# Kernel optimization log

Hardware: AMD Instinct MI355X
Metric: run time of the kernel (lower is better)

## Reference

```python
import jax, jax.numpy as jnp
import numpy as np

DIM = 768
CA = 192  # int(dim * mlp_ratio)
T = 8

def setup_inputs() -> dict:
    key = jax.random.key(0)
    ks = jax.random.split(key, 7)
    x = jax.random.normal(ks[0], (197, 128, DIM), dtype=jnp.float32)
    w1 = jax.random.normal(ks[1], (DIM, CA), dtype=jnp.float32) * 0.02
    b1 = jax.random.normal(ks[2], (CA,), dtype=jnp.float32) * 0.02
    conv_w = jax.random.normal(ks[3], (CA, 3), dtype=jnp.float32) * 0.02  # depthwise temporal kernel (3,1,1)
    conv_b = jax.random.normal(ks[4], (CA,), dtype=jnp.float32) * 0.02
    w2 = jax.random.normal(ks[5], (CA, DIM), dtype=jnp.float32) * 0.02
    b2 = jax.random.normal(ks[6], (DIM,), dtype=jnp.float32) * 0.02
    return {"x": x, "w1": w1, "b1": b1, "conv_w": conv_w, "conv_b": conv_b, "w2": w2, "b2": b2}

def reference(x, w1, b1, conv_w, conv_b, w2, b2):
    # x: (L, BT, dim), tokens-first layout (fc1 applied before permute)
    x_id = x
    h = x @ w1 + b1                      # (L, BT, Ca)
    h = jnp.transpose(h, (1, 0, 2))      # (BT, L, Ca)
    BT, L, Ca = h.shape
    B = BT // T
    h = h[:, 1:, :]                      # drop first token (L-1 patch tokens)
    x_cls = h[:, :1, :]                  # (BT, 1, Ca) -- first token AFTER the slice (as in original)
    x_temp = h.reshape(B, T, L - 1, Ca)  # (B, T, P, Ca)
    # Depthwise Conv3d with kernel (3,1,1), pad (1,0,0): pure temporal depthwise conv.
    xp = jnp.pad(x_temp, ((0, 0), (1, 1), (0, 0), (0, 0)))
    x_after = (xp[:, :-2] * conv_w[:, 0] + xp[:, 1:-1] * conv_w[:, 1]
               + xp[:, 2:] * conv_w[:, 2] + conv_b)  # (B, T, P, Ca)
    # Triangular-masked pairwise diff: sum_{i<j} (x_after[j] - x_temp[i]) / 28,
    # computed without materializing the (B,T,T,P,Ca) diff tensor:
    # each x_after[j] appears j times; each x_temp[i] appears (T-1-i) times.
    t = jnp.arange(T, dtype=x.dtype)
    result = (jnp.einsum('t,btpc->bpc', t, x_after)
              - jnp.einsum('t,btpc->bpc', (T - 1) - t, x_temp)) / 28.0
    x_last = (x_temp + result[:, None]).reshape(BT, L - 1, Ca)
    out = jnp.concatenate([x_cls, x_last], axis=1)   # (BT, L, Ca)
    out = jnp.transpose(out, (1, 0, 2))              # (L, BT, Ca)
    out = jax.nn.gelu(out, approximate=False)        # torch nn.GELU default = exact erf
    out = out @ w2 + b2                              # (L, BT, dim)
    return x_id + out
```

## Files before the change

### kernel.cpp

```cpp
#include <hip/hip_runtime.h>
#include <hip/hip_bf16.h>
#include <math.h>

#define DIM   768
#define CA    192
#define NTOK  25216

typedef __attribute__((ext_vector_type(8))) short short8;
typedef __attribute__((ext_vector_type(4))) float f32x4;

static __device__ __forceinline__ short f2bf(float f) {
    union { __hip_bfloat16 b; short s; } u;
    u.b = __float2bfloat16(f);
    return u.s;
}
static __device__ __forceinline__ float gelu_exact(float x) {
    return 0.5f * x * (1.0f + erff(x * 0.70710678118654752440f));
}
static __device__ __forceinline__ void ld16(void* lds, const void* gsrc) {
    __builtin_amdgcn_global_load_lds((const __attribute__((address_space(1))) void*)gsrc,
                                     (__attribute__((address_space(3))) void*)lds, 16, 0, 0);
}

__global__ void prep_kernel(const float* __restrict__ w1, const float* __restrict__ w2,
                            short* __restrict__ w1T, short* __restrict__ w2T) {
    int idx = blockIdx.x * 256 + threadIdx.x;
    if (idx < CA * DIM) {
        int n = idx / DIM, k = idx - n * DIM;
        w1T[idx] = f2bf(w1[k * CA + n]);
        int n2 = idx / CA, k2 = idx - n2 * CA;
        w2T[idx] = f2bf(w2[k2 * DIM + n2]);
    }
}

__global__ __launch_bounds__(256) void gemm1_fused(
        const float* __restrict__ x, const short* __restrict__ w1T,
        const float* __restrict__ b1, const float* __restrict__ conv_w,
        const float* __restrict__ conv_b, short* __restrict__ gq) {
    __shared__ __align__(16) short As[64 * 40];
    __shared__ __align__(16) short Bs[2][96 * 32];

    const int tid = threadIdx.x;
    const int bx  = blockIdx.x;
    const int l   = (bx >> 2) + 1;
    const int hm  = (bx >> 1) & 1;
    const int n0  = (bx & 1) * 96;
    const int R0  = l * 128 + hm * 64;

    const int wave = tid >> 6, lane = tid & 63;
    const int wm = wave >> 1, wn = wave & 1;
    const int lm = lane & 15, lg = lane >> 4;
    const int lk = lg * 8;

    const int arow = tid >> 2;
    const int acol = (tid & 3) * 8;
    const float* xrow = x + (size_t)(R0 + arow) * DIM + acol;

    f32x4 acc[2][3] = {};

    f32x4 av0 = *(const f32x4*)(xrow);
    f32x4 av1 = *(const f32x4*)(xrow + 4);
    if (wave < 3) {
        #pragma unroll
        for (int j = 0; j < 2; j++) {
            int s = (wave * 2 + j) * 64 + lane;
            int m = s >> 2;
            int q = (s & 3) ^ ((m >> 1) & 3);
            ld16(&Bs[0][(wave * 2 + j) * 512], w1T + (size_t)(n0 + m) * DIM + q * 8);
        }
    }

    for (int i = 0; i < 24; i++) {
        const int p = i & 1;
        short8 a8;
        #pragma unroll
        for (int e = 0; e < 4; e++) { a8[e] = f2bf(av0[e]); a8[4 + e] = f2bf(av1[e]); }
        __syncthreads();
        *(short8*)&As[arow * 40 + acol] = a8;
        __syncthreads();
        if (i < 23) {
            const float* xn = xrow + (i + 1) * 32;
            av0 = *(const f32x4*)(xn);
            av1 = *(const f32x4*)(xn + 4);
            if (wave < 3) {
                const int k0n = (i + 1) * 32;
                #pragma unroll
                for (int j = 0; j < 2; j++) {
                    int s = (wave * 2 + j) * 64 + lane;
                    int m = s >> 2;
                    int q = (s & 3) ^ ((m >> 1) & 3);
                    ld16(&Bs[1 - p][(wave * 2 + j) * 512],
                         w1T + (size_t)(n0 + m) * DIM + k0n + q * 8);
                }
            }
        }
        short8 af[2], bf[3];
        af[0] = *(const short8*)&As[(wm * 32 + lm) * 40 + lk];
        af[1] = *(const short8*)&As[(wm * 32 + 16 + lm) * 40 + lk];
        #pragma unroll
        for (int j = 0; j < 3; j++) {
            int rB = wn * 48 + j * 16 + lm;
            int qs = lg ^ ((rB >> 1) & 3);
            bf[j] = *(const short8*)&Bs[p][rB * 32 + qs * 8];
        }
        #pragma unroll
        for (int i2 = 0; i2 < 2; i2++)
            #pragma unroll
            for (int j = 0; j < 3; j++)
                acc[i2][j] = __builtin_amdgcn_mfma_f32_16x16x32_bf16(af[i2], bf[j], acc[i2][j], 0, 0, 0);
    }

    const int g1 = lg & 1;
    #pragma unroll
    for (int j = 0; j < 3; j++) {
        const int c = n0 + wn * 48 + j * 16 + lm;
        const float b1c = b1[c];
        const float cw0 = conv_w[c * 3 + 0];
        const float cw1 = conv_w[c * 3 + 1];
        const float cw2 = conv_w[c * 3 + 2];
        const float cb  = conv_b[c];
        #pragma unroll
        for (int i2 = 0; i2 < 2; i2++) {
            float hv[4];
            #pragma unroll
            for (int r = 0; r < 4; r++) hv[r] = acc[i2][j][r] + b1c;
            float partial = 0.f;
            #pragma unroll
            for (int r = 0; r < 4; r++) {
                const int t = g1 * 4 + r;
                const float tf = (float)t;
                float coef = tf * cw1 - (7.0f - tf);
                if (t <= 6) coef += (tf + 1.0f) * cw0;
                if (t >= 1) coef += (tf - 1.0f) * cw2;
                partial += coef * hv[r];
            }
            const float full = partial + __shfl_xor(partial, 16);
            const float res = cb + full * (1.0f / 28.0f);
            const int row = R0 + wm * 32 + i2 * 16 + lg * 4;
            #pragma unroll
            for (int r = 0; r < 4; r++)
                gq[(size_t)(row + r) * CA + c] = f2bf(gelu_exact(hv[r] + res));
            if (l == 1) {
                const int bt = row - 128;
                #pragma unroll
                for (int r = 0; r < 4; r++)
                    gq[(size_t)(bt + r) * CA + c] = f2bf(gelu_exact(hv[r]));
            }
        }
    }
}

__global__ __launch_bounds__(256) void gemm2_kernel(
        const short* __restrict__ gq, const short* __restrict__ w2T,
        const float* __restrict__ b2, const float* __restrict__ x,
        float* __restrict__ out) {
    __shared__ __align__(16) short As[2][64 * 64];
    __shared__ __align__(16) short Bs[2][128 * 64];

    const int tid = threadIdx.x;
    const int m0 = blockIdx.x * 64;
    const int n0 = blockIdx.y * 128;
    const int wave = tid >> 6, lane = tid & 63;
    const int wm = wave >> 1, wn = wave & 1;
    const int lm = lane & 15, lg = lane >> 4;

    f32x4 acc[2][4] = {};

    #pragma unroll
    for (int j = 0; j < 2; j++) {
        int s = (wave * 2 + j) * 64 + lane;
        int m = s >> 3, q = (s & 7) ^ (m & 7);
        ld16(&As[0][(wave * 2 + j) * 512], gq + (size_t)(m0 + m) * CA + q * 8);
    }
    #pragma unroll
    for (int j = 0; j < 4; j++) {
        int s = (wave * 4 + j) * 64 + lane;
        int m = s >> 3, q = (s & 7) ^ (m & 7);
        ld16(&Bs[0][(wave * 4 + j) * 512], w2T + (size_t)(n0 + m) * CA + q * 8);
    }

    for (int i = 0; i < 3; i++) {
        const int p = i & 1;
        __syncthreads();
        if (i < 2) {
            const int k0 = (i + 1) * 64;
            #pragma unroll
            for (int j = 0; j < 2; j++) {
                int s = (wave * 2 + j) * 64 + lane;
                int m = s >> 3, q = (s & 7) ^ (m & 7);
                ld16(&As[1 - p][(wave * 2 + j) * 512], gq + (size_t)(m0 + m) * CA + k0 + q * 8);
            }
            #pragma unroll
            for (int j = 0; j < 4; j++) {
                int s = (wave * 4 + j) * 64 + lane;
                int m = s >> 3, q = (s & 7) ^ (m & 7);
                ld16(&Bs[1 - p][(wave * 4 + j) * 512], w2T + (size_t)(n0 + m) * CA + k0 + q * 8);
            }
        }
        #pragma unroll
        for (int kk = 0; kk < 2; kk++) {
            const int cb0 = kk * 4 + lg;
            short8 af[2], bf[4];
            #pragma unroll
            for (int i2 = 0; i2 < 2; i2++) {
                int r = wm * 32 + i2 * 16 + lm;
                af[i2] = *(const short8*)&As[p][r * 64 + (cb0 ^ (r & 7)) * 8];
            }
            #pragma unroll
            for (int j = 0; j < 4; j++) {
                int r = wn * 64 + j * 16 + lm;
                bf[j] = *(const short8*)&Bs[p][r * 64 + (cb0 ^ (r & 7)) * 8];
            }
            #pragma unroll
            for (int i2 = 0; i2 < 2; i2++)
                #pragma unroll
                for (int j = 0; j < 4; j++)
                    acc[i2][j] = __builtin_amdgcn_mfma_f32_16x16x32_bf16(af[i2], bf[j], acc[i2][j], 0, 0, 0);
        }
    }

    #pragma unroll
    for (int i2 = 0; i2 < 2; i2++) {
        const int row0 = m0 + wm * 32 + i2 * 16 + lg * 4;
        #pragma unroll
        for (int j = 0; j < 4; j++) {
            const int col = n0 + wn * 64 + j * 16 + lm;
            const float bias = b2[col];
            #pragma unroll
            for (int r = 0; r < 4; r++) {
                const size_t idx = (size_t)(row0 + r) * DIM + col;
                out[idx] = acc[i2][j][r] + x[idx] + bias;
            }
        }
    }
}

extern "C" void kernel_launch(void* const* d_in, const int* in_sizes, int n_in,
                              void* d_out, int out_size, void* d_ws, size_t ws_size,
                              hipStream_t stream) {
    (void)in_sizes; (void)n_in; (void)out_size; (void)ws_size;
    const float* x      = (const float*)d_in[0];
    const float* w1     = (const float*)d_in[1];
    const float* b1     = (const float*)d_in[2];
    const float* conv_w = (const float*)d_in[3];
    const float* conv_b = (const float*)d_in[4];
    const float* w2     = (const float*)d_in[5];
    const float* b2     = (const float*)d_in[6];
    float* out = (float*)d_out;

    char* ws = (char*)d_ws;
    short* g   = (short*)ws;
    short* w1T = (short*)(ws + 9682944);
    short* w2T = (short*)(ws + 9682944 + 294912);

    prep_kernel<<<(CA * DIM + 255) / 256, 256, 0, stream>>>(w1, w2, w1T, w2T);
    gemm1_fused<<<784, 256, 0, stream>>>(x, w1T, b1, conv_w, conv_b, g);
    gemm2_kernel<<<dim3(394, 6), 256, 0, stream>>>(g, w2T, b2, x, out);
}
```

Baseline: 196.3 us.

## Load GEMM operands straight from global into registers, dropping LDS staging

Both GEMM kernels stop staging A and B tiles through shared memory with barriers. Each lane now loads its MFMA fragments directly from global memory into registers, prefetching the next k-step one iteration ahead, and launch bounds request 4 blocks per CU. This removes the LDS round trips and __syncthreads overhead, but each wave re-reads data that was previously shared across waves, which raises global/L2 traffic and uses less coalesced access patterns.

```diff
diff --git a/kernel.cpp b/kernel.cpp
--- a/kernel.cpp
+++ b/kernel.cpp
@@ -16,10 +16,6 @@
 }
 static __device__ __forceinline__ float gelu_exact(float x) {
     return 0.5f * x * (1.0f + erff(x * 0.70710678118654752440f));
-}
-static __device__ __forceinline__ void ld16(void* lds, const void* gsrc) {
-    __builtin_amdgcn_global_load_lds((const __attribute__((address_space(1))) void*)gsrc,
-                                     (__attribute__((address_space(3))) void*)lds, 16, 0, 0);
 }
 
 __global__ void prep_kernel(const float* __restrict__ w1, const float* __restrict__ w2,
@@ -33,13 +29,10 @@
     }
 }
 
-__global__ __launch_bounds__(256) void gemm1_fused(
+__global__ __launch_bounds__(256, 4) void gemm1_fused(
         const float* __restrict__ x, const short* __restrict__ w1T,
         const float* __restrict__ b1, const float* __restrict__ conv_w,
         const float* __restrict__ conv_b, short* __restrict__ gq) {
-    __shared__ __align__(16) short As[64 * 40];
-    __shared__ __align__(16) short Bs[2][96 * 32];
-
     const int tid = threadIdx.x;
     const int bx  = blockIdx.x;
     const int l   = (bx >> 2) + 1;
@@ -50,64 +43,68 @@
     const int wave = tid >> 6, lane = tid & 63;
     const int wm = wave >> 1, wn = wave & 1;
     const int lm = lane & 15, lg = lane >> 4;
-    const int lk = lg * 8;
-
-    const int arow = tid >> 2;
-    const int acol = (tid & 3) * 8;
-    const float* xrow = x + (size_t)(R0 + arow) * DIM + acol;
+
+    const float* aBase0 = x + (size_t)(R0 + wm * 32 + lm) * DIM + lg * 8;
+    const float* aBase1 = aBase0 + (size_t)16 * DIM;
+    const short* bBase  = w1T + (size_t)(n0 + wn * 48 + lm) * DIM + lg * 8;
 
     f32x4 acc[2][3] = {};
 
-    f32x4 av0 = *(const f32x4*)(xrow);
-    f32x4 av1 = *(const f32x4*)(xrow + 4);
-    if (wave < 3) {
-        #pragma unroll
-        for (int j = 0; j < 2; j++) {
-            int s = (wave * 2 + j) * 64 + lane;
-            int m = s >> 2;
-            int q = (s & 3) ^ ((m >> 1) & 3);
-            ld16(&Bs[0][(wave * 2 + j) * 512], w1T + (size_t)(n0 + m) * DIM + q * 8);
-        }
-    }
-
-    for (int i = 0; i < 24; i++) {
-        const int p = i & 1;
-        short8 a8;
-        #pragma unroll
-        for (int e = 0; e < 4; e++) { a8[e] = f2bf(av0[e]); a8[4 + e] = f2bf(av1[e]); }
-        __syncthreads();
-        *(short8*)&As[arow * 40 + acol] = a8;
-        __syncthreads();
-        if (i < 23) {
-            const float* xn = xrow + (i + 1) * 32;
-            av0 = *(const f32x4*)(xn);
-            av1 = *(const f32x4*)(xn + 4);
-            if (wave < 3) {
-                const int k0n = (i + 1) * 32;
-                #pragma unroll
-                for (int j = 0; j < 2; j++) {
-                    int s = (wave * 2 + j) * 64 + lane;
-                    int m = s >> 2;
-                    int q = (s & 3) ^ ((m >> 1) & 3);
-                    ld16(&Bs[1 - p][(wave * 2 + j) * 512],
-                         w1T + (size_t)(n0 + m) * DIM + k0n + q * 8);
-                }
-            }
-        }
-        short8 af[2], bf[3];
-        af[0] = *(const short8*)&As[(wm * 32 + lm) * 40 + lk];
-        af[1] = *(const short8*)&As[(wm * 32 + 16 + lm) * 40 + lk];
-        #pragma unroll
-        for (int j = 0; j < 3; j++) {
-            int rB = wn * 48 + j * 16 + lm;
-            int qs = lg ^ ((rB >> 1) & 3);
-            bf[j] = *(const short8*)&Bs[p][rB * 32 + qs * 8];
+    f32x4 pa[2][2];
+    short8 pb[3];
+    pa[0][0] = *(const f32x4*)(aBase0);
+    pa[0][1] = *(const f32x4*)(aBase0 + 4);
+    pa[1][0] = *(const f32x4*)(aBase1);
+    pa[1][1] = *(const f32x4*)(aBase1 + 4);
+    pb[0] = *(const short8*)(bBase);
+    pb[1] = *(const short8*)(bBase + 16 * DIM);
+    pb[2] = *(const short8*)(bBase + 32 * DIM);
+
+    #pragma unroll
+    for (int i = 0; i < 23; i++) {
+        const int kn = (i + 1) * 32;
+        f32x4 na[2][2];
+        short8 nb[3];
+        na[0][0] = *(const f32x4*)(aBase0 + kn);
+        na[0][1] = *(const f32x4*)(aBase0 + kn + 4);
+        na[1][0] = *(const f32x4*)(aBase1 + kn);
+        na[1][1] = *(const f32x4*)(aBase1 + kn + 4);
+        nb[0] = *(const short8*)(bBase + kn);
+        nb[1] = *(const short8*)(bBase + 16 * DIM + kn);
+        nb[2] = *(const short8*)(bBase + 32 * DIM + kn);
+
+        short8 af[2];
+        #pragma unroll
+        for (int e = 0; e < 4; e++) {
+            af[0][e]     = f2bf(pa[0][0][e]);
+            af[0][4 + e] = f2bf(pa[0][1][e]);
+            af[1][e]     = f2bf(pa[1][0][e]);
+            af[1][4 + e] = f2bf(pa[1][1][e]);
         }
         #pragma unroll
         for (int i2 = 0; i2 < 2; i2++)
             #pragma unroll
             for (int j = 0; j < 3; j++)
-                acc[i2][j] = __builtin_amdgcn_mfma_f32_16x16x32_bf16(af[i2], bf[j], acc[i2][j], 0, 0, 0);
+                acc[i2][j] = __builtin_amdgcn_mfma_f32_16x16x32_bf16(af[i2], pb[j], acc[i2][j], 0, 0, 0);
+
+        pa[0][0] = na[0][0]; pa[0][1] = na[0][1];
+        pa[1][0] = na[1][0]; pa[1][1] = na[1][1];
+        pb[0] = nb[0]; pb[1] = nb[1]; pb[2] = nb[2];
+    }
+    {
+        short8 af[2];
+        #pragma unroll
+        for (int e = 0; e < 4; e++) {
+            af[0][e]     = f2bf(pa[0][0][e]);
+            af[0][4 + e] = f2bf(pa[0][1][e]);
+            af[1][e]     = f2bf(pa[1][0][e]);
+            af[1][4 + e] = f2bf(pa[1][1][e]);
+        }
+        #pragma unroll
+        for (int i2 = 0; i2 < 2; i2++)
+            #pragma unroll
+            for (int j = 0; j < 3; j++)
+                acc[i2][j] = __builtin_amdgcn_mfma_f32_16x16x32_bf16(af[i2], pb[j], acc[i2][j], 0, 0, 0);
     }
 
     const int g1 = lg & 1;
@@ -150,13 +147,10 @@
     }
 }
 
-__global__ __launch_bounds__(256) void gemm2_kernel(
+__global__ __launch_bounds__(256, 4) void gemm2_kernel(
         const short* __restrict__ gq, const short* __restrict__ w2T,
         const float* __restrict__ b2, const float* __restrict__ x,
         float* __restrict__ out) {
-    __shared__ __align__(16) short As[2][64 * 64];
-    __shared__ __align__(16) short Bs[2][128 * 64];
-
     const int tid = threadIdx.x;
     const int m0 = blockIdx.x * 64;
     const int n0 = blockIdx.y * 128;
@@ -164,60 +158,44 @@
     const int wm = wave >> 1, wn = wave & 1;
     const int lm = lane & 15, lg = lane >> 4;
 
+    const short* aBase = gq  + (size_t)(m0 + wm * 32 + lm) * CA + lg * 8;
+    const short* bBase = w2T + (size_t)(n0 + wn * 64 + lm) * CA + lg * 8;
+
     f32x4 acc[2][4] = {};
 
-    #pragma unroll
-    for (int j = 0; j < 2; j++) {
-        int s = (wave * 2 + j) * 64 + lane;
-        int m = s >> 3, q = (s & 7) ^ (m & 7);
-        ld16(&As[0][(wave * 2 + j) * 512], gq + (size_t)(m0 + m) * CA + q * 8);
-    }
-    #pragma unroll
-    for (int j = 0; j < 4; j++) {
-        int s = (wave * 4 + j) * 64 + lane;
-        int m = s >> 3, q = (s & 7) ^ (m & 7);
-        ld16(&Bs[0][(wave * 4 + j) * 512], w2T + (size_t)(n0 + m) * CA + q * 8);
-    }
-
-    for (int i = 0; i < 3; i++) {
-        const int p = i & 1;
-        __syncthreads();
-        if (i < 2) {
-            const int k0 = (i + 1) * 64;
-            #pragma unroll
-            for (int j = 0; j < 2; j++) {
-                int s = (wave * 2 + j) * 64 + lane;
-                int m = s >> 3, q = (s & 7) ^ (m & 7);
-                ld16(&As[1 - p][(wave * 2 + j) * 512], gq + (size_t)(m0 + m) * CA + k0 + q * 8);
-            }
-            #pragma unroll
-            for (int j = 0; j < 4; j++) {
-                int s = (wave * 4 + j) * 64 + lane;
-                int m = s >> 3, q = (s & 7) ^ (m & 7);
-                ld16(&Bs[1 - p][(wave * 4 + j) * 512], w2T + (size_t)(n0 + m) * CA + k0 + q * 8);
-            }
-        }
-        #pragma unroll
-        for (int kk = 0; kk < 2; kk++) {
-            const int cb0 = kk * 4 + lg;
-            short8 af[2], bf[4];
-            #pragma unroll
-            for (int i2 = 0; i2 < 2; i2++) {
-                int r = wm * 32 + i2 * 16 + lm;
-                af[i2] = *(const short8*)&As[p][r * 64 + (cb0 ^ (r & 7)) * 8];
-            }
-            #pragma unroll
-            for (int j = 0; j < 4; j++) {
-                int r = wn * 64 + j * 16 + lm;
-                bf[j] = *(const short8*)&Bs[p][r * 64 + (cb0 ^ (r & 7)) * 8];
-            }
-            #pragma unroll
-            for (int i2 = 0; i2 < 2; i2++)
-                #pragma unroll
-                for (int j = 0; j < 4; j++)
-                    acc[i2][j] = __builtin_amdgcn_mfma_f32_16x16x32_bf16(af[i2], bf[j], acc[i2][j], 0, 0, 0);
-        }
-    }
+    short8 pa[2], pb[4];
+    pa[0] = *(const short8*)(aBase);
+    pa[1] = *(const short8*)(aBase + 16 * CA);
+    pb[0] = *(const short8*)(bBase);
+    pb[1] = *(const short8*)(bBase + 16 * CA);
+    pb[2] = *(const short8*)(bBase + 32 * CA);
+    pb[3] = *(const short8*)(bBase + 48 * CA);
+
+    #pragma unroll
+    for (int i = 0; i < 5; i++) {
+        const int kn = (i + 1) * 32;
+        short8 na[2], nb[4];
+        na[0] = *(const short8*)(aBase + kn);
+        na[1] = *(const short8*)(aBase + 16 * CA + kn);
+        nb[0] = *(const short8*)(bBase + kn);
+        nb[1] = *(const short8*)(bBase + 16 * CA + kn);
+        nb[2] = *(const short8*)(bBase + 32 * CA + kn);
+        nb[3] = *(const short8*)(bBase + 48 * CA + kn);
+
+        #pragma unroll
+        for (int i2 = 0; i2 < 2; i2++)
+            #pragma unroll
+            for (int j = 0; j < 4; j++)
+                acc[i2][j] = __builtin_amdgcn_mfma_f32_16x16x32_bf16(pa[i2], pb[j], acc[i2][j], 0, 0, 0);
+
+        pa[0] = na[0]; pa[1] = na[1];
+        pb[0] = nb[0]; pb[1] = nb[1]; pb[2] = nb[2]; pb[3] = nb[3];
+    }
+    #pragma unroll
+    for (int i2 = 0; i2 < 2; i2++)
+        #pragma unroll
+        for (int j = 0; j < 4; j++)
+            acc[i2][j] = __builtin_amdgcn_mfma_f32_16x16x32_bf16(pa[i2], pb[j], acc[i2][j], 0, 0, 0);
 
     #pragma unroll
     for (int i2 = 0; i2 < 2; i2++) {
```

Result: slower. 255.4 us (+30.1%).

## Pre-convert x to bf16 and triple-buffer gemm1 with async LDS loads

Applied to the files above, without the earlier changes.

Adds a separate pass that converts x to bf16 into the output buffer, used as scratch. gemm1 can then stage both A and B tiles with global_load_lds in a 3-stage ring, using K=64 steps and fine-grained vmcnt waits. This replaces the in-register fp32->bf16 conversion and the double syncthreads per step. gemm2 gets a unified LDS ring with per-wave load assignment and a launch-bounds occupancy hint of 2. The cost is an extra full read of x and a write of a bf16 copy before gemm1, in exchange for better latency hiding.

```diff
diff --git a/kernel.cpp b/kernel.cpp
--- a/kernel.cpp
+++ b/kernel.cpp
@@ -33,12 +33,22 @@
     }
 }
 
-__global__ __launch_bounds__(256) void gemm1_fused(
-        const float* __restrict__ x, const short* __restrict__ w1T,
+__global__ __launch_bounds__(256) void xcvt_kernel(const float* __restrict__ x,
+                                                   short* __restrict__ xbf) {
+    size_t i = ((size_t)blockIdx.x * 256 + threadIdx.x) * 8;
+    f32x4 a = *(const f32x4*)(x + i);
+    f32x4 b = *(const f32x4*)(x + i + 4);
+    short8 o;
+    #pragma unroll
+    for (int e = 0; e < 4; e++) { o[e] = f2bf(a[e]); o[4 + e] = f2bf(b[e]); }
+    *(short8*)(xbf + i) = o;
+}
+
+__global__ __launch_bounds__(256, 2) void gemm1_fused(
+        const short* __restrict__ xbf, const short* __restrict__ w1T,
         const float* __restrict__ b1, const float* __restrict__ conv_w,
         const float* __restrict__ conv_b, short* __restrict__ gq) {
-    __shared__ __align__(16) short As[64 * 40];
-    __shared__ __align__(16) short Bs[2][96 * 32];
+    __shared__ __align__(16) short lds[3][10240];
 
     const int tid = threadIdx.x;
     const int bx  = blockIdx.x;
@@ -50,64 +60,71 @@
     const int wave = tid >> 6, lane = tid & 63;
     const int wm = wave >> 1, wn = wave & 1;
     const int lm = lane & 15, lg = lane >> 4;
-    const int lk = lg * 8;
-
-    const int arow = tid >> 2;
-    const int acol = (tid & 3) * 8;
-    const float* xrow = x + (size_t)(R0 + arow) * DIM + acol;
+
+    const short* src[5];
+    int loff[5];
+    #pragma unroll
+    for (int j = 0; j < 5; j++) {
+        int s5 = wave * 5 + j;
+        if (s5 < 8) {
+            int idx = s5 * 64 + lane;
+            int m = idx >> 3, q = (idx & 7) ^ (m & 7);
+            src[j]  = xbf + (size_t)(R0 + m) * DIM + q * 8;
+            loff[j] = s5 * 512;
+        } else {
+            int idx = (s5 - 8) * 64 + lane;
+            int m = idx >> 3, q = (idx & 7) ^ (m & 7);
+            src[j]  = w1T + (size_t)(n0 + m) * DIM + q * 8;
+            loff[j] = 4096 + (s5 - 8) * 512;
+        }
+    }
 
     f32x4 acc[2][3] = {};
 
-    f32x4 av0 = *(const f32x4*)(xrow);
-    f32x4 av1 = *(const f32x4*)(xrow + 4);
-    if (wave < 3) {
-        #pragma unroll
-        for (int j = 0; j < 2; j++) {
-            int s = (wave * 2 + j) * 64 + lane;
-            int m = s >> 2;
-            int q = (s & 3) ^ ((m >> 1) & 3);
-            ld16(&Bs[0][(wave * 2 + j) * 512], w1T + (size_t)(n0 + m) * DIM + q * 8);
-        }
-    }
-
-    for (int i = 0; i < 24; i++) {
-        const int p = i & 1;
-        short8 a8;
-        #pragma unroll
-        for (int e = 0; e < 4; e++) { a8[e] = f2bf(av0[e]); a8[4 + e] = f2bf(av1[e]); }
-        __syncthreads();
-        *(short8*)&As[arow * 40 + acol] = a8;
-        __syncthreads();
-        if (i < 23) {
-            const float* xn = xrow + (i + 1) * 32;
-            av0 = *(const f32x4*)(xn);
-            av1 = *(const f32x4*)(xn + 4);
-            if (wave < 3) {
-                const int k0n = (i + 1) * 32;
-                #pragma unroll
-                for (int j = 0; j < 2; j++) {
-                    int s = (wave * 2 + j) * 64 + lane;
-                    int m = s >> 2;
-                    int q = (s & 3) ^ ((m >> 1) & 3);
-                    ld16(&Bs[1 - p][(wave * 2 + j) * 512],
-                         w1T + (size_t)(n0 + m) * DIM + k0n + q * 8);
-                }
-            }
-        }
-        short8 af[2], bf[3];
-        af[0] = *(const short8*)&As[(wm * 32 + lm) * 40 + lk];
-        af[1] = *(const short8*)&As[(wm * 32 + 16 + lm) * 40 + lk];
+    auto STAGE = [&](int t, int buf) {
+        #pragma unroll
+        for (int j = 0; j < 5; j++)
+            ld16(&lds[buf][loff[j]], src[j] + t * 64);
+    };
+
+    STAGE(0, 0);
+    STAGE(1, 1);
+
+    #pragma unroll
+    for (int t = 0; t < 12; t++) {
+        if (t < 11) asm volatile("s_waitcnt vmcnt(5)" ::: "memory");
+        else        asm volatile("s_waitcnt vmcnt(0)" ::: "memory");
+        __builtin_amdgcn_s_barrier();
+        if (t < 10) STAGE(t + 2, (t + 2) % 3);
+
+        const short* A = &lds[t % 3][0];
+        const short* B = &lds[t % 3][4096];
+        short8 af[2][2], bf[3][2];
+        #pragma unroll
+        for (int i2 = 0; i2 < 2; i2++) {
+            int r = wm * 32 + i2 * 16 + lm;
+            #pragma unroll
+            for (int ks = 0; ks < 2; ks++) {
+                int c = ks * 4 + lg;
+                af[i2][ks] = *(const short8*)&A[(r * 8 + (c ^ (r & 7))) * 8];
+            }
+        }
         #pragma unroll
         for (int j = 0; j < 3; j++) {
             int rB = wn * 48 + j * 16 + lm;
-            int qs = lg ^ ((rB >> 1) & 3);
-            bf[j] = *(const short8*)&Bs[p][rB * 32 + qs * 8];
-        }
-        #pragma unroll
-        for (int i2 = 0; i2 < 2; i2++)
-            #pragma unroll
-            for (int j = 0; j < 3; j++)
-                acc[i2][j] = __builtin_amdgcn_mfma_f32_16x16x32_bf16(af[i2], bf[j], acc[i2][j], 0, 0, 0);
+            #pragma unroll
+            for (int ks = 0; ks < 2; ks++) {
+                int c = ks * 4 + lg;
+                bf[j][ks] = *(const short8*)&B[(rB * 8 + (c ^ (rB & 7))) * 8];
+            }
+        }
+        #pragma unroll
+        for (int ks = 0; ks < 2; ks++)
+            #pragma unroll
+            for (int i2 = 0; i2 < 2; i2++)
+                #pragma unroll
+                for (int j = 0; j < 3; j++)
+                    acc[i2][j] = __builtin_amdgcn_mfma_f32_16x16x32_bf16(af[i2][ks], bf[j][ks], acc[i2][j], 0, 0, 0);
     }
 
     const int g1 = lg & 1;
@@ -150,12 +167,11 @@
     }
 }
 
-__global__ __launch_bounds__(256) void gemm2_kernel(
+__global__ __launch_bounds__(256, 2) void gemm2_kernel(
         const short* __restrict__ gq, const short* __restrict__ w2T,
         const float* __restrict__ b2, const float* __restrict__ x,
         float* __restrict__ out) {
-    __shared__ __align__(16) short As[2][64 * 64];
-    __shared__ __align__(16) short Bs[2][128 * 64];
+    __shared__ __align__(16) short lds[2][12288];
 
     const int tid = threadIdx.x;
     const int m0 = blockIdx.x * 64;
@@ -164,52 +180,55 @@
     const int wm = wave >> 1, wn = wave & 1;
     const int lm = lane & 15, lg = lane >> 4;
 
+    const short* src[6];
+    int loff[6];
+    #pragma unroll
+    for (int j = 0; j < 6; j++) {
+        int s6 = wave * 6 + j;
+        if (s6 < 8) {
+            int idx = s6 * 64 + lane;
+            int m = idx >> 3, q = (idx & 7) ^ (m & 7);
+            src[j]  = gq + (size_t)(m0 + m) * CA + q * 8;
+            loff[j] = s6 * 512;
+        } else {
+            int idx = (s6 - 8) * 64 + lane;
+            int m = idx >> 3, q = (idx & 7) ^ (m & 7);
+            src[j]  = w2T + (size_t)(n0 + m) * CA + q * 8;
+            loff[j] = 4096 + (s6 - 8) * 512;
+        }
+    }
+
     f32x4 acc[2][4] = {};
 
-    #pragma unroll
-    for (int j = 0; j < 2; j++) {
-        int s = (wave * 2 + j) * 64 + lane;
-        int m = s >> 3, q = (s & 7) ^ (m & 7);
-        ld16(&As[0][(wave * 2 + j) * 512], gq + (size_t)(m0 + m) * CA + q * 8);
-    }
-    #pragma unroll
-    for (int j = 0; j < 4; j++) {
-        int s = (wave * 4 + j) * 64 + lane;
-        int m = s >> 3, q = (s & 7) ^ (m & 7);
-        ld16(&Bs[0][(wave * 4 + j) * 512], w2T + (size_t)(n0 + m) * CA + q * 8);
-    }
-
-    for (int i = 0; i < 3; i++) {
-        const int p = i & 1;
-        __syncthreads();
-        if (i < 2) {
-            const int k0 = (i + 1) * 64;
-            #pragma unroll
-            for (int j = 0; j < 2; j++) {
-                int s = (wave * 2 + j) * 64 + lane;
-                int m = s >> 3, q = (s & 7) ^ (m & 7);
-                ld16(&As[1 - p][(wave * 2 + j) * 512], gq + (size_t)(m0 + m) * CA + k0 + q * 8);
-            }
-            #pragma unroll
-            for (int j = 0; j < 4; j++) {
-                int s = (wave * 4 + j) * 64 + lane;
-                int m = s >> 3, q = (s & 7) ^ (m & 7);
-                ld16(&Bs[1 - p][(wave * 4 + j) * 512], w2T + (size_t)(n0 + m) * CA + k0 + q * 8);
-            }
-        }
+    auto STAGE = [&](int t, int buf) {
+        #pragma unroll
+        for (int j = 0; j < 6; j++)
+            ld16(&lds[buf][loff[j]], src[j] + t * 64);
+    };
+
+    STAGE(0, 0);
+
+    #pragma unroll
+    for (int t = 0; t < 3; t++) {
+        asm volatile("s_waitcnt vmcnt(0)" ::: "memory");
+        __builtin_amdgcn_s_barrier();
+        if (t < 2) STAGE(t + 1, (t + 1) & 1);
+
+        const short* A = &lds[t & 1][0];
+        const short* B = &lds[t & 1][4096];
         #pragma unroll
         for (int kk = 0; kk < 2; kk++) {
-            const int cb0 = kk * 4 + lg;
+            const int c = kk * 4 + lg;
             short8 af[2], bf[4];
             #pragma unroll
             for (int i2 = 0; i2 < 2; i2++) {
                 int r = wm * 32 + i2 * 16 + lm;
-                af[i2] = *(const short8*)&As[p][r * 64 + (cb0 ^ (r & 7)) * 8];
+                af[i2] = *(const short8*)&A[(r * 8 + (c ^ (r & 7))) * 8];
             }
             #pragma unroll
             for (int j = 0; j < 4; j++) {
-                int r = wn * 64 + j * 16 + lm;
-                bf[j] = *(const short8*)&Bs[p][r * 64 + (cb0 ^ (r & 7)) * 8];
+                int rB = wn * 64 + j * 16 + lm;
+                bf[j] = *(const short8*)&B[(rB * 8 + (c ^ (rB & 7))) * 8];
             }
             #pragma unroll
             for (int i2 = 0; i2 < 2; i2++)
@@ -252,8 +271,10 @@
     short* g   = (short*)ws;
     short* w1T = (short*)(ws + 9682944);
     short* w2T = (short*)(ws + 9682944 + 294912);
+    short* xbf = (short*)out;
 
     prep_kernel<<<(CA * DIM + 255) / 256, 256, 0, stream>>>(w1, w2, w1T, w2T);
-    gemm1_fused<<<784, 256, 0, stream>>>(x, w1T, b1, conv_w, conv_b, g);
+    xcvt_kernel<<<9456, 256, 0, stream>>>(x, xbf);
+    gemm1_fused<<<784, 256, 0, stream>>>(xbf, w1T, b1, conv_w, conv_b, g);
     gemm2_kernel<<<dim3(394, 6), 256, 0, stream>>>(g, w2T, b2, x, out);
 }
```

Result: slower. 201.9 us (+2.8%).
